# Kernel tuning notes

Hardware: AMD Instinct MI355X
Metric: run time of the kernel (lower is better)

## Reference

```python
import jax, jax.numpy as jnp
import numpy as np

D_MODEL = 1024
NUM_HEADS_Q = 16
NUM_HEADS_KV = 1
D_HEAD = D_MODEL // NUM_HEADS_Q  # 64
KV_DIM = D_HEAD * NUM_HEADS_KV   # 64


def setup_inputs() -> dict:
    key = jax.random.key(0)
    ks = jax.random.split(key, 9)
    b, n = 4, 2048
    s_in = 1.0 / np.sqrt(D_MODEL)
    s_o = 1.0 / np.sqrt(D_MODEL)
    return {
        "x": jax.random.normal(ks[0], (b, n, D_MODEL), jnp.float32),
        # weights stored as [in, out] (= torch Linear weight transposed)
        "W_q": jax.random.uniform(ks[1], (D_MODEL, D_MODEL), jnp.float32, -s_in, s_in),
        "b_q": jax.random.uniform(ks[2], (D_MODEL,), jnp.float32, -s_in, s_in),
        "W_k": jax.random.uniform(ks[3], (D_MODEL, KV_DIM), jnp.float32, -s_in, s_in),
        "b_k": jax.random.uniform(ks[4], (KV_DIM,), jnp.float32, -s_in, s_in),
        "W_v": jax.random.uniform(ks[5], (D_MODEL, KV_DIM), jnp.float32, -s_in, s_in),
        "b_v": jax.random.uniform(ks[6], (KV_DIM,), jnp.float32, -s_in, s_in),
        "W_o": jax.random.uniform(ks[7], (D_MODEL, D_MODEL), jnp.float32, -s_o, s_o),
        "b_o": jax.random.uniform(ks[8], (D_MODEL,), jnp.float32, -s_o, s_o),
    }


def reference(x, W_q, b_q, W_k, b_k, W_v, b_v, W_o, b_o):
    b, n, d_model = x.shape
    # projections
    q = (x @ W_q + b_q).reshape(b, n, NUM_HEADS_Q, D_HEAD).transpose(0, 2, 1, 3)  # [b,hq,n,dh]
    k = (x @ W_k + b_k).reshape(b, n, NUM_HEADS_KV, D_HEAD).transpose(0, 2, 1, 3)  # [b,hkv,n,dh]
    v = (x @ W_v + b_v).reshape(b, n, NUM_HEADS_KV, D_HEAD).transpose(0, 2, 1, 3)
    # MQA: single KV head broadcast over query heads via einsum broadcasting
    scale = 1.0 / np.sqrt(D_HEAD).astype(np.float32)
    # scores [b,hq,n,n]; k/v have hkv=1, broadcast over hq
    scores = jnp.einsum("bhqd,bknd->bhqn", q, k)[..., 0, :, :][:, :, None] if False else None
    # cleaner: squeeze kv head (num_heads_kv == 1)
    k1 = k[:, 0]  # [b,n,dh]
    v1 = v[:, 0]  # [b,n,dh]
    scores = jnp.einsum("bhqd,bkd->bhqk", q, k1) * scale  # [b,hq,n,n]
    attn = jax.nn.softmax(scores, axis=-1)
    out = jnp.einsum("bhqk,bkd->bhqd", attn, v1)  # [b,hq,n,dh]
    out = out.transpose(0, 2, 1, 3).reshape(b, n, d_model)
    return out @ W_o + b_o
```

## Files before the change

### kernel.cpp

```cpp
#include <hip/hip_runtime.h>

using bf16x8 = __attribute__((ext_vector_type(8))) short;
using f32x4  = __attribute__((ext_vector_type(4))) float;
using f32x16 = __attribute__((ext_vector_type(16))) float;
using u32x2  = __attribute__((ext_vector_type(2))) unsigned int;
using u32x4  = __attribute__((ext_vector_type(4))) unsigned int;

__device__ __forceinline__ unsigned short f2bf(float f) {
  unsigned int u = __float_as_uint(f);
  u = u + 0x7fffu + ((u >> 16) & 1u);
  return (unsigned short)(u >> 16);
}

#if __has_builtin(__builtin_amdgcn_exp2f)
#define EXP2(x) __builtin_amdgcn_exp2f(x)
#else
#define EXP2(x) __expf((x) * 0.69314718056f)
#endif

__device__ __forceinline__ unsigned int cvt_pk_bf16(float lo, float hi) {
  unsigned int r;
  asm("v_cvt_pk_bf16_f32 %0, %1, %2" : "=v"(r) : "v"(lo), "v"(hi));
  return r;
}

#define GLL16(SRC, DST) __builtin_amdgcn_global_load_lds( \
    (const __attribute__((address_space(1))) unsigned int*)(SRC), \
    (__attribute__((address_space(3))) unsigned int*)(DST), 16, 0, 0)

__global__ __launch_bounds__(256) void cvt_all_kernel(
    const float* __restrict__ x, unsigned short* __restrict__ xb,
    const float* __restrict__ Wq, const float* __restrict__ Wk,
    const float* __restrict__ Wv, const float* __restrict__ Wo,
    unsigned short* __restrict__ wqkvt, unsigned short* __restrict__ wot) {
  __shared__ float tile[32][33];
  const int bx = blockIdx.x;
  if (bx < 8192) {
    const int i = bx * 256 + threadIdx.x;
    const float4 v = reinterpret_cast<const float4*>(x)[i];
    ushort2 o0 = { f2bf(v.x), f2bf(v.y) };
    ushort2 o1 = { f2bf(v.z), f2bf(v.w) };
    reinterpret_cast<ushort2*>(xb)[2 * i]     = o0;
    reinterpret_cast<ushort2*>(xb)[2 * i + 1] = o1;
    return;
  }
  const float* W; unsigned short* Wt; int N, bi;
  if (bx < 9216)      { W = Wq; Wt = wqkvt;                        N = 1024; bi = bx - 8192; }
  else if (bx < 9280) { W = Wk; Wt = wqkvt + (size_t)1024 * 1024;  N = 64;   bi = bx - 9216; }
  else if (bx < 9344) { W = Wv; Wt = wqkvt + (size_t)1088 * 1024;  N = 64;   bi = bx - 9280; }
  else                { W = Wo; Wt = wot;                          N = 1024; bi = bx - 9344; }
  const int nb = N >> 5;
  const int n0 = (bi % nb) * 32, k0 = (bi / nb) * 32;
  const int tx = threadIdx.x & 31, ty = threadIdx.x >> 5;
  #pragma unroll
  for (int i = 0; i < 32; i += 8)
    tile[ty + i][tx] = W[(size_t)(k0 + ty + i) * N + n0 + tx];
  __syncthreads();
  #pragma unroll
  for (int i = 0; i < 32; i += 8)
    Wt[(size_t)(n0 + ty + i) * 1024 + k0 + tx] = f2bf(tile[tx][ty + i]);
}

template<int MODE>
__global__ __launch_bounds__(256) void gemm_kernel(
    const unsigned short* __restrict__ A, const unsigned short* __restrict__ Bt,
    const float* __restrict__ bias0, const float* __restrict__ bias1,
    const float* __restrict__ bias2,
    void* __restrict__ out0, void* __restrict__ out1, void* __restrict__ out2,
    int K, int N) {
  __shared__ __align__(16) unsigned short alds[2][128 * 32];
  __shared__ __align__(16) unsigned short blds[2][128 * 32];

  const int t    = threadIdx.x;
  const int lane = t & 63;
  const int wid  = t >> 6;
  const int lr = lane & 15, lg = lane >> 4;
  const int row0 = blockIdx.x * 128;
  const int col0 = blockIdx.y * 128;

  const size_t ldb = (size_t)K * 2;
  const char* Ag = (const char*)A  + (size_t)(row0 + (t >> 2)) * ldb + ((t & 3) << 4);
  const char* Bg = (const char*)Bt + (size_t)(col0 + (t >> 2)) * ldb + ((t & 3) << 4);
  char* adst = (char*)alds[0] + wid * 1024;
  char* bdst = (char*)blds[0] + wid * 1024;

  auto stage = [&](int buf, int k0) {
    const size_t kb = (size_t)k0 * 2;
    #pragma unroll
    for (int c = 0; c < 2; ++c) {
      GLL16(Ag + (size_t)c * 64 * ldb + kb, adst + buf * 8192 + c * 4096);
      GLL16(Bg + (size_t)c * 64 * ldb + kb, bdst + buf * 8192 + c * 4096);
    }
  };

  f32x4 acc[4][4];
  #pragma unroll
  for (int i = 0; i < 4; ++i)
    #pragma unroll
    for (int j = 0; j < 4; ++j)
      #pragma unroll
      for (int r = 0; r < 4; ++r) acc[i][j][r] = 0.f;

  stage(0, 0);
  __syncthreads();

  for (int step = 0; step < 32; ++step) {
    const int cur = step & 1;
    if (step < 31) stage(cur ^ 1, (step + 1) * 32);

    const char* ab = (const char*)alds[cur] + (wid >> 1) * 4096;
    const char* bb = (const char*)blds[cur] + (wid & 1) * 4096;
    bf16x8 am[4], bn[4];
    #pragma unroll
    for (int i = 0; i < 4; ++i)
      am[i] = *reinterpret_cast<const bf16x8*>(ab + (i * 16 + lr) * 64 + lg * 16);
    #pragma unroll
    for (int j = 0; j < 4; ++j)
      bn[j] = *reinterpret_cast<const bf16x8*>(bb + (j * 16 + lr) * 64 + lg * 16);
    #pragma unroll
    for (int i = 0; i < 4; ++i)
      #pragma unroll
      for (int j = 0; j < 4; ++j)
        acc[i][j] = __builtin_amdgcn_mfma_f32_16x16x32_bf16(am[i], bn[j], acc[i][j], 0, 0, 0);

    __syncthreads();
  }

  const int wrow0 = row0 + (wid >> 1) * 64;
  const int wcol0 = col0 + (wid & 1) * 64;
  #pragma unroll
  for (int i = 0; i < 4; ++i) {
    #pragma unroll
    for (int j = 0; j < 4; ++j) {
      const int col = wcol0 + j * 16 + lr;
      float bias;
      if constexpr (MODE == 0)
        bias = (col < 1024) ? bias0[col] : ((col < 1088) ? bias1[col - 1024] : bias2[col - 1088]);
      else
        bias = bias0[col];
      #pragma unroll
      for (int r = 0; r < 4; ++r) {
        const int row = wrow0 + i * 16 + lg * 4 + r;
        float v = acc[i][j][r] + bias;
        if constexpr (MODE == 0) {
          const int b = row >> 11, n = row & 2047;
          if (col < 1024) {
            v *= 0.180336880111f;
            const int h = col >> 6, d = col & 63;
            ((unsigned short*)out0)[(((b * 16 + h) * 2048) + n) * 64 + d] = f2bf(v);
          } else if (col < 1088) {
            ((unsigned short*)out1)[row * 64 + (col - 1024)] = f2bf(v);
          } else {
            const int np = (n & ~15) | (n & 3) | ((n & 4) << 1) | ((n & 8) >> 1);
            ((unsigned short*)out2)[(b * 64 + (col - 1088)) * 2048 + np] = f2bf(v);
          }
        } else {
          ((float*)out0)[(size_t)row * N + col] = v;
        }
      }
    }
  }
}

__global__ __launch_bounds__(256, 2) void attn_kernel(
    const unsigned short* __restrict__ Q,
    const unsigned short* __restrict__ Kb,
    const unsigned short* __restrict__ Vt,
    unsigned short* __restrict__ Ao) {
  __shared__ __align__(16) unsigned short klds[2][64 * 64];
  __shared__ __align__(16) unsigned short vlds[2][64 * 64];

  const int lane = threadIdx.x & 63;
  const int wid  = threadIdx.x >> 6;
  const int la = lane & 31, hi = lane >> 5;
  const int swz = (la & 7) << 4;
  const int bh = blockIdx.y, b = bh >> 4, h = bh & 15;
  const int q0 = blockIdx.x * 256 + wid * 64;

  const unsigned short* Qb = Q + (size_t)bh * 2048 * 64;
  const char* Kbase = (const char*)(Kb + (size_t)b * 2048 * 64);
  const char* Vbase = (const char*)(Vt + (size_t)b * 64 * 2048);

  const int srow  = lane >> 3;
  const int schnk = (lane & 7) ^ srow;
  const int koff0 = (wid * 16 + 0 + srow) * 128  + schnk * 16;
  const int koff1 = (wid * 16 + 8 + srow) * 128  + schnk * 16;
  const int voff0 = (wid * 16 + 0 + srow) * 4096 + schnk * 16;
  const int voff1 = (wid * 16 + 8 + srow) * 4096 + schnk * 16;
  char* kdst = (char*)klds[0] + wid * 2048;
  char* vdst = (char*)vlds[0] + wid * 2048;

  auto stage = [&](int buf, int kt) {
    GLL16(Kbase + (size_t)kt * 8192 + koff0, kdst + buf * 8192);
    GLL16(Kbase + (size_t)kt * 8192 + koff1, kdst + buf * 8192 + 1024);
    GLL16(Vbase + (size_t)kt * 128  + voff0, vdst + buf * 8192);
    GLL16(Vbase + (size_t)kt * 128  + voff1, vdst + buf * 8192 + 1024);
  };

  bf16x8 qa[2][4];
  #pragma unroll
  for (int qg = 0; qg < 2; ++qg)
    #pragma unroll
    for (int kc = 0; kc < 4; ++kc)
      qa[qg][kc] = *reinterpret_cast<const bf16x8*>(
          &Qb[(q0 + qg * 32 + la) * 64 + kc * 16 + hi * 8]);

  float lsum[2] = {0.f, 0.f};
  f32x16 o[2][2];
  #pragma unroll
  for (int qg = 0; qg < 2; ++qg)
    #pragma unroll
    for (int dt = 0; dt < 2; ++dt)
      #pragma unroll
      for (int r = 0; r < 16; ++r) o[qg][dt][r] = 0.f;

  auto body = [&](const char* kb8, const char* vb8) {
    #pragma unroll
    for (int ct = 0; ct < 2; ++ct) {
      f32x16 s0, s1;
      #pragma unroll
      for (int r = 0; r < 16; ++r) { s0[r] = 0.f; s1[r] = 0.f; }
      __builtin_amdgcn_s_setprio(1);
      #pragma unroll
      for (int kc = 0; kc < 4; ++kc) {
        const bf16x8 kf = *reinterpret_cast<const bf16x8*>(
            kb8 + ((ct * 32 + la) << 7) + ((((kc << 1) + hi) << 4) ^ swz));
        s0 = __builtin_amdgcn_mfma_f32_32x32x16_bf16(kf, qa[0][kc], s0, 0, 0, 0);
        s1 = __builtin_amdgcn_mfma_f32_32x32x16_bf16(kf, qa[1][kc], s1, 0, 0, 0);
      }
      __builtin_amdgcn_s_setprio(0);

      unsigned int W0[4][2], W1[4][2];
      float ps0 = 0.f, ps1 = 0.f;
      #pragma unroll
      for (int r2 = 0; r2 < 4; ++r2) {
        const float a0 = EXP2(s0[r2 * 4 + 0]), a1 = EXP2(s0[r2 * 4 + 1]);
        const float a2 = EXP2(s0[r2 * 4 + 2]), a3 = EXP2(s0[r2 * 4 + 3]);
        ps0 += (a0 + a1) + (a2 + a3);
        W0[r2][0] = cvt_pk_bf16(a0, a1);
        W0[r2][1] = cvt_pk_bf16(a2, a3);
        const float c0 = EXP2(s1[r2 * 4 + 0]), c1 = EXP2(s1[r2 * 4 + 1]);
        const float c2 = EXP2(s1[r2 * 4 + 2]), c3 = EXP2(s1[r2 * 4 + 3]);
        ps1 += (c0 + c1) + (c2 + c3);
        W1[r2][0] = cvt_pk_bf16(c0, c1);
        W1[r2][1] = cvt_pk_bf16(c2, c3);
      }
      lsum[0] += ps0;
      lsum[1] += ps1;

      __builtin_amdgcn_s_setprio(1);
      #pragma unroll
      for (int ks = 0; ks < 2; ++ks) {
        u32x4 w0, w1;
        w0[0] = W0[2 * ks][0]; w0[1] = W0[2 * ks][1];
        w0[2] = W0[2 * ks + 1][0]; w0[3] = W0[2 * ks + 1][1];
        w1[0] = W1[2 * ks][0]; w1[1] = W1[2 * ks][1];
        w1[2] = W1[2 * ks + 1][0]; w1[3] = W1[2 * ks + 1][1];
        const bf16x8 pb0 = __builtin_bit_cast(bf16x8, w0);
        const bf16x8 pb1 = __builtin_bit_cast(bf16x8, w1);
        #pragma unroll
        for (int dt = 0; dt < 2; ++dt) {
          const bf16x8 vf = *reinterpret_cast<const bf16x8*>(
              vb8 + ((dt * 32 + la) << 7) + (((((ct * 2 + ks) << 1) + hi) << 4) ^ swz));
          o[0][dt] = __builtin_amdgcn_mfma_f32_32x32x16_bf16(vf, pb0, o[0][dt], 0, 0, 0);
          o[1][dt] = __builtin_amdgcn_mfma_f32_32x32x16_bf16(vf, pb1, o[1][dt], 0, 0, 0);
        }
      }
      __builtin_amdgcn_s_setprio(0);
    }
  };

  stage(0, 0);
  __syncthreads();

  #pragma unroll 1
  for (int t2 = 0; t2 < 16; ++t2) {
    stage(1, 2 * t2 + 1);
    body((const char*)klds[0], (const char*)vlds[0]);
    __syncthreads();
    if (t2 < 15) stage(0, 2 * t2 + 2);
    body((const char*)klds[1], (const char*)vlds[1]);
    __syncthreads();
  }

  #pragma unroll
  for (int qg = 0; qg < 2; ++qg) {
    float l = lsum[qg];
    l += __shfl_xor(l, 32);
    const float inv = 1.f / l;
    const size_t rowoff = (size_t)(b * 2048 + q0 + qg * 32 + la) * 1024 + h * 64 + hi * 4;
    #pragma unroll
    for (int dt = 0; dt < 2; ++dt) {
      #pragma unroll
      for (int r2 = 0; r2 < 4; ++r2) {
        u32x2 w;
        w[0] = cvt_pk_bf16(o[qg][dt][r2 * 4 + 0] * inv, o[qg][dt][r2 * 4 + 1] * inv);
        w[1] = cvt_pk_bf16(o[qg][dt][r2 * 4 + 2] * inv, o[qg][dt][r2 * 4 + 3] * inv);
        *(u32x2*)(Ao + rowoff + dt * 32 + r2 * 8) = w;
      }
    }
  }
}

extern "C" void kernel_launch(void* const* d_in, const int* in_sizes, int n_in,
                              void* d_out, int out_size, void* d_ws, size_t ws_size,
                              hipStream_t stream) {
  const float* x  = (const float*)d_in[0];
  const float* Wq = (const float*)d_in[1];
  const float* bq = (const float*)d_in[2];
  const float* Wk = (const float*)d_in[3];
  const float* bk = (const float*)d_in[4];
  const float* Wv = (const float*)d_in[5];
  const float* bv = (const float*)d_in[6];
  const float* Wo = (const float*)d_in[7];
  const float* bo = (const float*)d_in[8];
  float* out = (float*)d_out;

  char* ws = (char*)d_ws;
  size_t off = 0;
  auto alloc = [&](size_t bytes) -> void* {
    void* p = ws + off;
    off += (bytes + 255) & ~(size_t)255;
    return p;
  };
  unsigned short* xb    = (unsigned short*)alloc((size_t)8192 * 1024 * 2);
  unsigned short* wqkvt = (unsigned short*)alloc((size_t)1152 * 1024 * 2);
  unsigned short* wot   = (unsigned short*)alloc((size_t)1024 * 1024 * 2);
  unsigned short* qb    = (unsigned short*)alloc((size_t)8192 * 1024 * 2);
  unsigned short* kb    = (unsigned short*)alloc((size_t)8192 * 64 * 2);
  unsigned short* vt    = (unsigned short*)alloc((size_t)4 * 64 * 2048 * 2);
  unsigned short* ao    = (unsigned short*)alloc((size_t)8192 * 1024 * 2);

  cvt_all_kernel<<<10368, 256, 0, stream>>>(x, xb, Wq, Wk, Wv, Wo, wqkvt, wot);
  gemm_kernel<0><<<dim3(64, 9), 256, 0, stream>>>(xb, wqkvt, bq, bk, bv, qb, kb, vt, 1024, 1152);
  attn_kernel<<<dim3(8, 64), 256, 0, stream>>>(qb, kb, vt, ao);
  gemm_kernel<2><<<dim3(64, 8), 256, 0, stream>>>(ao, wot, bo, nullptr, nullptr, out, nullptr, nullptr, 1024, 1024);
}
```

Baseline: 150.6 us.

## Load K/V fragments directly from global into registers, dropping LDS staging

Removes the shared-memory double buffer and block-wide barriers in the attention kernel. Each wave now loads its K and V MFMA fragments straight from global memory into registers, with register double-buffering across 32-key chunks. This is meant to cut LDS traffic and __syncthreads stalls. In exchange, every wave re-reads the shared K/V tiles from global/L2 (four times per block), issues more global loads, and uses more registers.

```diff
diff --git a/kernel.cpp b/kernel.cpp
--- a/kernel.cpp
+++ b/kernel.cpp
@@ -167,35 +167,15 @@
     const unsigned short* __restrict__ Kb,
     const unsigned short* __restrict__ Vt,
     unsigned short* __restrict__ Ao) {
-  __shared__ __align__(16) unsigned short klds[2][64 * 64];
-  __shared__ __align__(16) unsigned short vlds[2][64 * 64];
-
   const int lane = threadIdx.x & 63;
   const int wid  = threadIdx.x >> 6;
   const int la = lane & 31, hi = lane >> 5;
-  const int swz = (la & 7) << 4;
   const int bh = blockIdx.y, b = bh >> 4, h = bh & 15;
   const int q0 = blockIdx.x * 256 + wid * 64;
 
-  const unsigned short* Qb = Q + (size_t)bh * 2048 * 64;
-  const char* Kbase = (const char*)(Kb + (size_t)b * 2048 * 64);
-  const char* Vbase = (const char*)(Vt + (size_t)b * 64 * 2048);
-
-  const int srow  = lane >> 3;
-  const int schnk = (lane & 7) ^ srow;
-  const int koff0 = (wid * 16 + 0 + srow) * 128  + schnk * 16;
-  const int koff1 = (wid * 16 + 8 + srow) * 128  + schnk * 16;
-  const int voff0 = (wid * 16 + 0 + srow) * 4096 + schnk * 16;
-  const int voff1 = (wid * 16 + 8 + srow) * 4096 + schnk * 16;
-  char* kdst = (char*)klds[0] + wid * 2048;
-  char* vdst = (char*)vlds[0] + wid * 2048;
-
-  auto stage = [&](int buf, int kt) {
-    GLL16(Kbase + (size_t)kt * 8192 + koff0, kdst + buf * 8192);
-    GLL16(Kbase + (size_t)kt * 8192 + koff1, kdst + buf * 8192 + 1024);
-    GLL16(Vbase + (size_t)kt * 128  + voff0, vdst + buf * 8192);
-    GLL16(Vbase + (size_t)kt * 128  + voff1, vdst + buf * 8192 + 1024);
-  };
+  const unsigned short* Qb  = Q  + (size_t)bh * 2048 * 64;
+  const unsigned short* Kbb = Kb + (size_t)b * 2048 * 64;
+  const unsigned short* Vtb = Vt + (size_t)b * 64 * 2048;
 
   bf16x8 qa[2][4];
   #pragma unroll
@@ -214,73 +194,78 @@
       #pragma unroll
       for (int r = 0; r < 16; ++r) o[qg][dt][r] = 0.f;
 
-  auto body = [&](const char* kb8, const char* vb8) {
-    #pragma unroll
-    for (int ct = 0; ct < 2; ++ct) {
-      f32x16 s0, s1;
-      #pragma unroll
-      for (int r = 0; r < 16; ++r) { s0[r] = 0.f; s1[r] = 0.f; }
-      __builtin_amdgcn_s_setprio(1);
-      #pragma unroll
-      for (int kc = 0; kc < 4; ++kc) {
-        const bf16x8 kf = *reinterpret_cast<const bf16x8*>(
-            kb8 + ((ct * 32 + la) << 7) + ((((kc << 1) + hi) << 4) ^ swz));
-        s0 = __builtin_amdgcn_mfma_f32_32x32x16_bf16(kf, qa[0][kc], s0, 0, 0, 0);
-        s1 = __builtin_amdgcn_mfma_f32_32x32x16_bf16(kf, qa[1][kc], s1, 0, 0, 0);
+  auto loadK = [&](int c32, bf16x8 (&kf)[4]) {
+    const unsigned short* base = Kbb + (size_t)(c32 * 32 + la) * 64 + hi * 8;
+    #pragma unroll
+    for (int kc = 0; kc < 4; ++kc)
+      kf[kc] = *reinterpret_cast<const bf16x8*>(base + kc * 16);
+  };
+  auto loadV = [&](int c32, bf16x8 (&vf)[4]) {
+    #pragma unroll
+    for (int ks = 0; ks < 2; ++ks)
+      #pragma unroll
+      for (int dt = 0; dt < 2; ++dt)
+        vf[ks * 2 + dt] = *reinterpret_cast<const bf16x8*>(
+            Vtb + (size_t)(dt * 32 + la) * 2048 + c32 * 32 + ks * 16 + hi * 8);
+  };
+
+  auto compute = [&](const bf16x8 (&kf)[4], const bf16x8 (&vf)[4]) {
+    f32x16 s0, s1;
+    #pragma unroll
+    for (int r = 0; r < 16; ++r) { s0[r] = 0.f; s1[r] = 0.f; }
+    __builtin_amdgcn_s_setprio(1);
+    #pragma unroll
+    for (int kc = 0; kc < 4; ++kc) {
+      s0 = __builtin_amdgcn_mfma_f32_32x32x16_bf16(kf[kc], qa[0][kc], s0, 0, 0, 0);
+      s1 = __builtin_amdgcn_mfma_f32_32x32x16_bf16(kf[kc], qa[1][kc], s1, 0, 0, 0);
+    }
+    __builtin_amdgcn_s_setprio(0);
+
+    unsigned int W0[4][2], W1[4][2];
+    float ps0 = 0.f, ps1 = 0.f;
+    #pragma unroll
+    for (int r2 = 0; r2 < 4; ++r2) {
+      const float a0 = EXP2(s0[r2 * 4 + 0]), a1 = EXP2(s0[r2 * 4 + 1]);
+      const float a2 = EXP2(s0[r2 * 4 + 2]), a3 = EXP2(s0[r2 * 4 + 3]);
+      ps0 += (a0 + a1) + (a2 + a3);
+      W0[r2][0] = cvt_pk_bf16(a0, a1);
+      W0[r2][1] = cvt_pk_bf16(a2, a3);
+      const float c0 = EXP2(s1[r2 * 4 + 0]), c1 = EXP2(s1[r2 * 4 + 1]);
+      const float c2 = EXP2(s1[r2 * 4 + 2]), c3 = EXP2(s1[r2 * 4 + 3]);
+      ps1 += (c0 + c1) + (c2 + c3);
+      W1[r2][0] = cvt_pk_bf16(c0, c1);
+      W1[r2][1] = cvt_pk_bf16(c2, c3);
+    }
+    lsum[0] += ps0;
+    lsum[1] += ps1;
+
+    __builtin_amdgcn_s_setprio(1);
+    #pragma unroll
+    for (int ks = 0; ks < 2; ++ks) {
+      u32x4 w0, w1;
+      w0[0] = W0[2 * ks][0]; w0[1] = W0[2 * ks][1];
+      w0[2] = W0[2 * ks + 1][0]; w0[3] = W0[2 * ks + 1][1];
+      w1[0] = W1[2 * ks][0]; w1[1] = W1[2 * ks][1];
+      w1[2] = W1[2 * ks + 1][0]; w1[3] = W1[2 * ks + 1][1];
+      const bf16x8 pb0 = __builtin_bit_cast(bf16x8, w0);
+      const bf16x8 pb1 = __builtin_bit_cast(bf16x8, w1);
+      #pragma unroll
+      for (int dt = 0; dt < 2; ++dt) {
+        o[0][dt] = __builtin_amdgcn_mfma_f32_32x32x16_bf16(vf[ks * 2 + dt], pb0, o[0][dt], 0, 0, 0);
+        o[1][dt] = __builtin_amdgcn_mfma_f32_32x32x16_bf16(vf[ks * 2 + dt], pb1, o[1][dt], 0, 0, 0);
       }
-      __builtin_amdgcn_s_setprio(0);
-
-      unsigned int W0[4][2], W1[4][2];
-      float ps0 = 0.f, ps1 = 0.f;
-      #pragma unroll
-      for (int r2 = 0; r2 < 4; ++r2) {
-        const float a0 = EXP2(s0[r2 * 4 + 0]), a1 = EXP2(s0[r2 * 4 + 1]);
-        const float a2 = EXP2(s0[r2 * 4 + 2]), a3 = EXP2(s0[r2 * 4 + 3]);
-        ps0 += (a0 + a1) + (a2 + a3);
-        W0[r2][0] = cvt_pk_bf16(a0, a1);
-        W0[r2][1] = cvt_pk_bf16(a2, a3);
-        const float c0 = EXP2(s1[r2 * 4 + 0]), c1 = EXP2(s1[r2 * 4 + 1]);
-        const float c2 = EXP2(s1[r2 * 4 + 2]), c3 = EXP2(s1[r2 * 4 + 3]);
-        ps1 += (c0 + c1) + (c2 + c3);
-        W1[r2][0] = cvt_pk_bf16(c0, c1);
-        W1[r2][1] = cvt_pk_bf16(c2, c3);
-      }
-      lsum[0] += ps0;
-      lsum[1] += ps1;
-
-      __builtin_amdgcn_s_setprio(1);
-      #pragma unroll
-      for (int ks = 0; ks < 2; ++ks) {
-        u32x4 w0, w1;
-        w0[0] = W0[2 * ks][0]; w0[1] = W0[2 * ks][1];
-        w0[2] = W0[2 * ks + 1][0]; w0[3] = W0[2 * ks + 1][1];
-        w1[0] = W1[2 * ks][0]; w1[1] = W1[2 * ks][1];
-        w1[2] = W1[2 * ks + 1][0]; w1[3] = W1[2 * ks + 1][1];
-        const bf16x8 pb0 = __builtin_bit_cast(bf16x8, w0);
-        const bf16x8 pb1 = __builtin_bit_cast(bf16x8, w1);
-        #pragma unroll
-        for (int dt = 0; dt < 2; ++dt) {
-          const bf16x8 vf = *reinterpret_cast<const bf16x8*>(
-              vb8 + ((dt * 32 + la) << 7) + (((((ct * 2 + ks) << 1) + hi) << 4) ^ swz));
-          o[0][dt] = __builtin_amdgcn_mfma_f32_32x32x16_bf16(vf, pb0, o[0][dt], 0, 0, 0);
-          o[1][dt] = __builtin_amdgcn_mfma_f32_32x32x16_bf16(vf, pb1, o[1][dt], 0, 0, 0);
-        }
-      }
-      __builtin_amdgcn_s_setprio(0);
-    }
-  };
-
-  stage(0, 0);
-  __syncthreads();
-
+    }
+    __builtin_amdgcn_s_setprio(0);
+  };
+
+  bf16x8 kA[4], vA[4], kB[4], vB[4];
+  loadK(0, kA); loadV(0, vA);
   #pragma unroll 1
-  for (int t2 = 0; t2 < 16; ++t2) {
-    stage(1, 2 * t2 + 1);
-    body((const char*)klds[0], (const char*)vlds[0]);
-    __syncthreads();
-    if (t2 < 15) stage(0, 2 * t2 + 2);
-    body((const char*)klds[1], (const char*)vlds[1]);
-    __syncthreads();
+  for (int c2 = 0; c2 < 32; ++c2) {
+    loadK(2 * c2 + 1, kB); loadV(2 * c2 + 1, vB);
+    compute(kA, vA);
+    if (c2 < 31) { loadK(2 * c2 + 2, kA); loadV(2 * c2 + 2, vA); }
+    compute(kB, vB);
   }
 
   #pragma unroll
```

Result: slower. 204.4 us (+35.8%).
